# Performance work log

Hardware: AMD Instinct MI355X
Metric: run time of the kernel (lower is better)

Reference implementation:

```python
import jax, jax.numpy as jnp
import numpy as np

D_MODEL = 1024
D_HEAD = 64
N_HEADS = D_MODEL // D_HEAD
MAX_SEQ = 2048
BATCH = 2
SEQ = 2048


def setup_inputs() -> dict:
    key = jax.random.key(0)
    ks = jax.random.split(key, 10)
    s = 1.0 / np.sqrt(D_MODEL)
    return {
        "x": jax.random.normal(ks[0], (BATCH, SEQ, D_MODEL), dtype=jnp.float32),
        "Wq": jax.random.normal(ks[1], (D_MODEL, D_MODEL), dtype=jnp.float32) * s,
        "bq": jax.random.normal(ks[2], (D_MODEL,), dtype=jnp.float32) * 0.01,
        "Wk": jax.random.normal(ks[3], (D_MODEL, D_MODEL), dtype=jnp.float32) * s,
        "bk": jax.random.normal(ks[4], (D_MODEL,), dtype=jnp.float32) * 0.01,
        "Wv": jax.random.normal(ks[5], (D_MODEL, D_MODEL), dtype=jnp.float32) * s,
        "bv": jax.random.normal(ks[6], (D_MODEL,), dtype=jnp.float32) * 0.01,
        "Er": jax.random.normal(ks[7], (MAX_SEQ, D_HEAD), dtype=jnp.float32),
        "Wo": jax.random.normal(ks[8], (D_MODEL, D_MODEL), dtype=jnp.float32) * s,
        "bo": jax.random.normal(ks[9], (D_MODEL,), dtype=jnp.float32) * 0.01,
    }


def _s_rel(q, Er):
    # q: [B,H,S,Dh]; use last S rows of Er (start = max_seq - seq)
    S = q.shape[2]
    Er_slice = Er[Er.shape[0] - S:, :]                  # [S, Dh]
    qE = jnp.einsum("bhsd,ld->bhsl", q, Er_slice)       # [B,H,S,S]
    padded = jnp.pad(qE, ((0, 0), (0, 0), (0, 0), (1, 0)))  # [B,H,S,S+1]
    B, H, S1, S2 = padded.shape
    padded = padded.reshape(B, H, S2, S1)               # skew trick
    return padded[:, :, 1:, :]                          # [B,H,S,S]


def reference(x, Wq, bq, Wk, bk, Wv, bv, Er, Wo, bo):
    B, S, _ = x.shape
    scale = 1.0 / np.sqrt(D_HEAD)
    # projections (torch Linear: x @ W.T + b)
    def proj(W, b):
        return (x @ W.T + b).reshape(B, S, N_HEADS, D_HEAD).transpose(0, 2, 1, 3)
    q = proj(Wq, bq)   # [B,H,S,Dh]
    k = proj(Wk, bk)
    v = proj(Wv, bv)
    qk = jnp.einsum("bhsd,bhtd->bhst", q, k)            # [B,H,S,S]
    logits = (qk + _s_rel(q, Er)) * scale
    causal = jnp.tril(jnp.ones((S, S), dtype=bool))
    masked = jnp.where(causal[None, None], logits, -1e9)
    attn = jax.nn.softmax(masked, axis=-1)
    out = jnp.einsum("bhst,bhtd->bhsd", attn, v)        # [B,H,S,Dh]
    out = out.transpose(0, 2, 1, 3).reshape(B, S, D_MODEL)
    return out @ Wo.T + bo
```

## Files before the change

kernel.cpp:

```cpp
#include <hip/hip_runtime.h>
#include <hip/hip_bf16.h>

typedef short v8s __attribute__((ext_vector_type(8)));
typedef float v4f __attribute__((ext_vector_type(4)));
typedef __hip_bfloat16 bf16;
typedef unsigned int u32;

#define MFMA(a, b, c) __builtin_amdgcn_mfma_f32_16x16x32_bf16(a, b, c, 0, 0, 0)

__device__ __forceinline__ void gload16(const bf16* g, bf16* l) {
    __builtin_amdgcn_global_load_lds(
        (const __attribute__((address_space(1))) u32*)(g),
        (__attribute__((address_space(3))) u32*)(l), 16, 0, 0);
}

__global__ __launch_bounds__(256) void cast_all(
    const float* __restrict__ x,  const float* __restrict__ wq,
    const float* __restrict__ wk, const float* __restrict__ wv,
    const float* __restrict__ wo, const float* __restrict__ er,
    bf16* __restrict__ xb,  bf16* __restrict__ wqb, bf16* __restrict__ wkb,
    bf16* __restrict__ wvb, bf16* __restrict__ wob, bf16* __restrict__ erb)
{
    const int r = blockIdx.y;
    const float* s; bf16* d; int n4;
    if      (r == 0) { s = x;  d = xb;  n4 = 1048576; }
    else if (r == 1) { s = wq; d = wqb; n4 = 262144;  }
    else if (r == 2) { s = wk; d = wkb; n4 = 262144;  }
    else if (r == 3) { s = wv; d = wvb; n4 = 262144;  }
    else if (r == 4) { s = wo; d = wob; n4 = 262144;  }
    else             { s = er; d = erb; n4 = 32768;   }
    const int i = blockIdx.x * 256 + threadIdx.x;
    if (i < n4) {
        const float4 v = ((const float4*)s)[i];
        bf16 t[4];
        t[0] = __float2bfloat16(v.x);
        t[1] = __float2bfloat16(v.y);
        t[2] = __float2bfloat16(v.z);
        t[3] = __float2bfloat16(v.w);
        ((uint2*)d)[i] = *(const uint2*)t;
    }
}

__global__ __launch_bounds__(256) void gemm_nt(
    const bf16* __restrict__ A, const bf16* __restrict__ W,
    const float* __restrict__ b0, const float* __restrict__ b1,
    const float* __restrict__ b2,
    bf16* __restrict__ oHM, bf16* __restrict__ Vt, float* __restrict__ outf)
{
    __shared__ bf16 As[2][128 * 64];
    __shared__ bf16 Bs[2][128 * 64];

    const int tid = threadIdx.x;
    const int w  = tid >> 6, l = tid & 63;
    const int lm = l & 15,  lq = l >> 4;
    const int wm = (w >> 1) * 64, wn = (w & 1) * 64;
    const int m0 = blockIdx.y * 128, n0 = blockIdx.x * 128;

    const int grow = l >> 3;
    const int gcol = ((l & 7) ^ grow) * 8;

    v4f acc[4][4];
#pragma unroll
    for (int i = 0; i < 4; ++i)
#pragma unroll
        for (int j = 0; j < 4; ++j) acc[i][j] = (v4f){0.f, 0.f, 0.f, 0.f};

    const int sw = (lm & 7) << 4;

    auto STAGE = [&](int p, int k0) {
#pragma unroll
        for (int q = 0; q < 4; ++q) {
            const int rr = w * 32 + q * 8;
            gload16(&A[(size_t)(m0 + rr + grow) * 1024 + k0 + gcol], &As[p][rr * 64]);
            gload16(&W[(size_t)(n0 + rr + grow) * 1024 + k0 + gcol], &Bs[p][rr * 64]);
        }
    };
    auto COMPUTE = [&](int p) {
#pragma unroll
        for (int kk = 0; kk < 2; ++kk) {
            v8s a[4], b[4];
            const int cb = (lq * 16 + kk * 64);
#pragma unroll
            for (int i = 0; i < 4; ++i) {
                const int row = wm + i * 16 + lm;
                a[i] = *(const v8s*)((const char*)As[p] + row * 128 + (cb ^ sw));
            }
#pragma unroll
            for (int j = 0; j < 4; ++j) {
                const int row = wn + j * 16 + lm;
                b[j] = *(const v8s*)((const char*)Bs[p] + row * 128 + (cb ^ sw));
            }
#pragma unroll
            for (int i = 0; i < 4; ++i)
#pragma unroll
                for (int j = 0; j < 4; ++j)
                    acc[i][j] = MFMA(b[j], a[i], acc[i][j]);
        }
    };

    STAGE(0, 0);
    __syncthreads();
    for (int t = 0; t < 15; ++t) {
        STAGE((t + 1) & 1, (t + 1) * 64);
        COMPUTE(t & 1);
        __syncthreads();
    }
    COMPUTE(1);

    const int z = blockIdx.x >> 3;
    const float* bias = (z == 0) ? b0 : (z == 1) ? b1 : b2;

    float4 bj[4];
#pragma unroll
    for (int j = 0; j < 4; ++j)
        bj[j] = *(const float4*)&bias[(n0 & 1023) + wn + j * 16 + lq * 4];

#pragma unroll
    for (int i = 0; i < 4; ++i) {
        const int row = m0 + wm + i * 16 + lm;
        const int bb = row >> 11, ss = row & 2047;
#pragma unroll
        for (int j = 0; j < 4; ++j) {
            const int cc = (n0 & 1023) + wn + j * 16 + lq * 4;
            const float v0 = acc[i][j][0] + bj[j].x;
            const float v1 = acc[i][j][1] + bj[j].y;
            const float v2 = acc[i][j][2] + bj[j].z;
            const float v3 = acc[i][j][3] + bj[j].w;
            if (outf) {
                const float4 fv = {v0, v1, v2, v3};
                *(float4*)&outf[(size_t)row * 1024 + cc] = fv;
            } else {
                bf16 t[4];
                t[0] = __float2bfloat16(v0);
                t[1] = __float2bfloat16(v1);
                t[2] = __float2bfloat16(v2);
                t[3] = __float2bfloat16(v3);
                const int hh = cc >> 6, dd = cc & 63;
                if (z < 2) {
                    *(uint2*)&oHM[(size_t)z * 4194304 +
                        ((size_t)(bb * 16 + hh) * 2048 + ss) * 64 + dd] = *(uint2*)t;
                } else {
#pragma unroll
                    for (int r = 0; r < 4; ++r)
                        Vt[((size_t)(bb * 16 + hh) * 64 + dd + r) * 2048 + ss] = t[r];
                }
            }
        }
    }
}

__device__ const unsigned char QBt[48] = {
    31,31,30,15, 30,29,29,28,14, 28,27,27,26,13, 26,25,25,24,12,
    24,23,23,22,11, 22,21,21,20,10, 20,19,19,18,9, 18,17,17,16,8,
    16,7, 6,5,4,3,2,1,0};
__device__ const unsigned char TTt[48] = {
     0, 1, 0, 2,  1, 0, 1, 0, 2,  1, 0, 1, 0, 2,  1, 0, 1, 0, 2,
     1, 0, 1, 0, 2,  1, 0, 1, 0, 2,  1, 0, 1, 0, 2,  1, 0, 1, 0, 2,
     1, 2, 2,2,2,2,2,2,2};

__global__ __launch_bounds__(256, 4) void attn(
    const bf16* __restrict__ Q, const bf16* __restrict__ K,
    const bf16* __restrict__ Vt, const bf16* __restrict__ Er,
    bf16* __restrict__ AO, float* __restrict__ Opart, float* __restrict__ dpart)
{
    __shared__ bf16 Ks[64 * 72];
    __shared__ bf16 Vs[64 * 72];
    __shared__ bf16 Ps[64 * 72];
    __shared__ bf16 Gs2[64 * 100];

    const int ord = blockIdx.x;
    const int bh = ord & 31;
    const int s  = ord >> 5;
    const int qb = QBt[s];
    const int tt = TTt[s];
    const int t0   = (tt == 2) ? 0 : tt;
    const int step = (tt == 2) ? 1 : 2;
    const int slot = (tt == 2) ? -1 : (((qb - 16) * 32 + bh) * 2 + tt);

    const int i0 = qb * 64;
    const int b  = bh >> 4, h = bh & 15;
    const int tid = threadIdx.x;
    const int w  = tid >> 6, l = tid & 63;
    const int lm = l & 15,  lq = l >> 4;

    const bf16* qp = Q + ((size_t)bh * 2048 + i0 + w * 16 + lm) * 64 + lq * 8;
    const v8s q0 = *(const v8s*)qp;
    const v8s q1f = *(const v8s*)(qp + 32);

    v4f accO[4];
#pragma unroll
    for (int dt = 0; dt < 4; ++dt) accO[dt] = (v4f){0.f, 0.f, 0.f, 0.f};
    float rsc = 0.f;

    const int sr0 = tid >> 3;
    const int sc8 = (tid & 7) * 8;
    const size_t kbase = (size_t)bh * 2048 * 64;
    const size_t vbase = (size_t)bh * 64 * 2048;

    const int grow_g = (w * 16 + lm) * 100;
    const int prow   = (w * 16 + lm) * 72;
    const int ig     = i0 + w * 16 + lm;

    const int jt0 = t0 * 64;
    uint4 kp0 = *(const uint4*)&K[kbase + (size_t)(jt0 + sr0) * 64 + sc8];
    uint4 kp1 = *(const uint4*)&K[kbase + (size_t)(jt0 + sr0 + 32) * 64 + sc8];
    uint4 vp0 = *(const uint4*)&Vt[vbase + (size_t)sr0 * 2048 + jt0 + sc8];
    uint4 vp1 = *(const uint4*)&Vt[vbase + (size_t)(sr0 + 32) * 2048 + jt0 + sc8];

    for (int it = t0; it <= qb; it += step) {
        const int j0 = it * 64;
        __syncthreads();
        *(uint4*)&Ks[sr0 * 72 + sc8]        = kp0;
        *(uint4*)&Ks[(sr0 + 32) * 72 + sc8] = kp1;
        *(uint4*)&Vs[sr0 * 72 + sc8]        = vp0;
        *(uint4*)&Vs[(sr0 + 32) * 72 + sc8] = vp1;
        if (it + step <= qb) {
            const int jn = j0 + step * 64;
            kp0 = *(const uint4*)&K[kbase + (size_t)(jn + sr0) * 64 + sc8];
            kp1 = *(const uint4*)&K[kbase + (size_t)(jn + sr0 + 32) * 64 + sc8];
            vp0 = *(const uint4*)&Vt[vbase + (size_t)sr0 * 2048 + jn + sc8];
            vp1 = *(const uint4*)&Vt[vbase + (size_t)(sr0 + 32) * 2048 + jn + sc8];
        }
        const int basew = 2048 - 16 - i0 + j0 - 16 * w;
#pragma unroll
        for (int ct2 = 0; ct2 < 5; ++ct2) {
            int mr = basew + ct2 * 16 + lm;
            mr = (mr > 2047) ? 2047 : mr;
            const bf16* ep = Er + (size_t)mr * 64 + lq * 8;
            const v8s e0 = *(const v8s*)ep;
            const v8s e1 = *(const v8s*)(ep + 32);
            v4f g = (v4f){0.f, 0.f, 0.f, 0.f};
            g = MFMA(e0, q0, g);
            g = MFMA(e1, q1f, g);
            const int cb = ct2 * 16 + lq * 4 + lm + 1;
#pragma unroll
            for (int r = 0; r < 4; ++r)
                Gs2[grow_g + cb + r] = __float2bfloat16(g[r] * 0.125f);
        }
        __syncthreads();
        v4f sv[4];
#pragma unroll
        for (int ct = 0; ct < 4; ++ct) {
            const v8s k0f = *(const v8s*)&Ks[(ct * 16 + lm) * 72 + lq * 8];
            const v8s k1f = *(const v8s*)&Ks[(ct * 16 + lm) * 72 + 32 + lq * 8];
            v4f s2 = (v4f){0.f, 0.f, 0.f, 0.f};
            s2 = MFMA(k0f, q0, s2);
            s2 = MFMA(k1f, q1f, s2);
            sv[ct] = s2;
        }
#pragma unroll
        for (int ct = 0; ct < 4; ++ct) {
            const uint2 graw = *(const uint2*)&Gs2[grow_g + 16 + ct * 16 + lq * 4];
            const bf16* gb4 = (const bf16*)&graw;
            bf16 pt[4];
#pragma unroll
            for (int r = 0; r < 4; ++r) {
                const int jj = ct * 16 + lq * 4 + r;
                float sc = fmaf(sv[ct][r], 0.125f, (float)gb4[r]);
                if (j0 + jj > ig) sc = -1e9f;
                const float pe = __expf(sc - 4.0f);
                rsc += pe;
                pt[r] = __float2bfloat16(pe);
            }
            *(uint2*)&Ps[prow + ct * 16 + lq * 4] = *(const uint2*)pt;
        }
        const v8s pa0 = *(const v8s*)&Ps[prow + lq * 8];
        const v8s pa1 = *(const v8s*)&Ps[prow + 32 + lq * 8];
#pragma unroll
        for (int dt = 0; dt < 4; ++dt) {
            const v8s vb0 = *(const v8s*)&Vs[(dt * 16 + lm) * 72 + lq * 8];
            const v8s vb1 = *(const v8s*)&Vs[(dt * 16 + lm) * 72 + 32 + lq * 8];
            accO[dt] = MFMA(pa0, vb0, accO[dt]);
            accO[dt] = MFMA(pa1, vb1, accO[dt]);
        }
    }
    rsc += __shfl_xor(rsc, 16, 64);
    rsc += __shfl_xor(rsc, 32, 64);
    float den[4];
#pragma unroll
    for (int r = 0; r < 4; ++r) den[r] = __shfl(rsc, lq * 4 + r, 64);

    if (slot < 0) {
#pragma unroll
        for (int dt = 0; dt < 4; ++dt) {
#pragma unroll
            for (int r = 0; r < 4; ++r) {
                const int row = i0 + w * 16 + lq * 4 + r;
                const int d   = dt * 16 + lm;
                const float v = accO[dt][r] / den[r];
                AO[((size_t)b * 2048 + row) * 1024 + h * 64 + d] = __float2bfloat16(v);
            }
        }
    } else {
        float* op = Opart + (size_t)slot * 4096;
#pragma unroll
        for (int dt = 0; dt < 4; ++dt) {
#pragma unroll
            for (int r = 0; r < 4; ++r) {
                const int row = w * 16 + lq * 4 + r;
                op[row * 64 + dt * 16 + lm] = accO[dt][r];
            }
        }
        if (lm == 0) {
#pragma unroll
            for (int r = 0; r < 4; ++r)
                dpart[slot * 64 + w * 16 + lq * 4 + r] = den[r];
        }
    }
}

__global__ __launch_bounds__(256) void fixup(
    const float* __restrict__ Opart, const float* __restrict__ dpart,
    bf16* __restrict__ AO)
{
    const int pi = blockIdx.x;
    const int qb = 16 + (pi >> 5);
    const int bh = pi & 31;
    const int b = bh >> 4, h = bh & 15;
    const int t = threadIdx.x;
    const int row = t >> 2;
    const int c0 = (t & 3) * 16;
    const float dA = dpart[(pi * 2) * 64 + row];
    const float dB = dpart[(pi * 2 + 1) * 64 + row];
    const float inv = 1.0f / (dA + dB);
    const float* A = Opart + (size_t)(pi * 2) * 4096 + row * 64 + c0;
    const float* B = Opart + (size_t)(pi * 2 + 1) * 4096 + row * 64 + c0;
    bf16* dst = AO + ((size_t)b * 2048 + qb * 64 + row) * 1024 + h * 64 + c0;
#pragma unroll
    for (int c = 0; c < 16; c += 4) {
        bf16 tt[4];
#pragma unroll
        for (int r = 0; r < 4; ++r)
            tt[r] = __float2bfloat16((A[c + r] + B[c + r]) * inv);
        *(uint2*)&dst[c] = *(uint2*)tt;
    }
}

extern "C" void kernel_launch(void* const* d_in, const int* in_sizes, int n_in,
                              void* d_out, int out_size, void* d_ws, size_t ws_size,
                              hipStream_t stream)
{
    const float* x  = (const float*)d_in[0];
    const float* Wq = (const float*)d_in[1];
    const float* bq = (const float*)d_in[2];
    const float* Wk = (const float*)d_in[3];
    const float* bk = (const float*)d_in[4];
    const float* Wv = (const float*)d_in[5];
    const float* bv = (const float*)d_in[6];
    const float* Er = (const float*)d_in[7];
    const float* Wo = (const float*)d_in[8];
    const float* bo = (const float*)d_in[9];
    float* out = (float*)d_out;

    bf16* ws = (bf16*)d_ws;
    const size_t NEl = (size_t)4096 * 1024;
    bf16* Qw  = ws;
    bf16* Kw  = ws + NEl;
    bf16* Vtw = ws + 3 * NEl;
    bf16* xb  = ws + 4 * NEl;
    bf16* AOw = xb;
    bf16* Wqb = ws + 5 * NEl;
    bf16* Wkb = Wqb + 1024 * 1024;
    bf16* Wvb = Wkb + 1024 * 1024;
    bf16* Wob = Wvb + 1024 * 1024;
    bf16* Erb = Wob + 1024 * 1024;
    float* dpart = (float*)(Erb + (size_t)2048 * 64);
    float* Opart = out;
    (void)Kw;

    cast_all<<<dim3(4096, 6), 256, 0, stream>>>(x, Wq, Wk, Wv, Wo, Er,
                                                xb, Wqb, Wkb, Wvb, Wob, Erb);
    gemm_nt<<<dim3(24, 32), 256, 0, stream>>>(xb, Wqb, bq, bk, bv, Qw, Vtw, nullptr);
    attn<<<dim3(1536), 256, 0, stream>>>(Qw, Kw, Vtw, Erb, AOw, Opart, dpart);
    fixup<<<dim3(512), 256, 0, stream>>>(Opart, dpart, AOw);
    gemm_nt<<<dim3(8, 32), 256, 0, stream>>>(AOw, Wob, bo, bo, bo, nullptr, nullptr, out);
}
```

Baseline: 273.7 us.

## Read K and V fragments directly from global memory, drop LDS staging

Removes the K/V shared-memory tiles and their register prefetch, so each wave loads its MFMA operand fragments for K and Vt straight from global memory (served by cache). This frees LDS and registers and removes one barrier per iteration, and launch bounds are raised to allow 6 blocks per CU for more occupancy. The cost is that the four waves now each fetch the same K/V data redundantly through the cache hierarchy, and the loads are no longer prefetched one iteration ahead, so latency may be exposed.

```diff
diff --git a/kernel.cpp b/kernel.cpp
--- a/kernel.cpp
+++ b/kernel.cpp
@@ -158,13 +158,11 @@
      1, 0, 1, 0, 2,  1, 0, 1, 0, 2,  1, 0, 1, 0, 2,  1, 0, 1, 0, 2,
      1, 2, 2,2,2,2,2,2,2};
 
-__global__ __launch_bounds__(256, 4) void attn(
+__global__ __launch_bounds__(256, 6) void attn(
     const bf16* __restrict__ Q, const bf16* __restrict__ K,
     const bf16* __restrict__ Vt, const bf16* __restrict__ Er,
     bf16* __restrict__ AO, float* __restrict__ Opart, float* __restrict__ dpart)
 {
-    __shared__ bf16 Ks[64 * 72];
-    __shared__ bf16 Vs[64 * 72];
     __shared__ bf16 Ps[64 * 72];
     __shared__ bf16 Gs2[64 * 100];
 
@@ -192,8 +190,6 @@
     for (int dt = 0; dt < 4; ++dt) accO[dt] = (v4f){0.f, 0.f, 0.f, 0.f};
     float rsc = 0.f;
 
-    const int sr0 = tid >> 3;
-    const int sc8 = (tid & 7) * 8;
     const size_t kbase = (size_t)bh * 2048 * 64;
     const size_t vbase = (size_t)bh * 64 * 2048;
 
@@ -201,26 +197,8 @@
     const int prow   = (w * 16 + lm) * 72;
     const int ig     = i0 + w * 16 + lm;
 
-    const int jt0 = t0 * 64;
-    uint4 kp0 = *(const uint4*)&K[kbase + (size_t)(jt0 + sr0) * 64 + sc8];
-    uint4 kp1 = *(const uint4*)&K[kbase + (size_t)(jt0 + sr0 + 32) * 64 + sc8];
-    uint4 vp0 = *(const uint4*)&Vt[vbase + (size_t)sr0 * 2048 + jt0 + sc8];
-    uint4 vp1 = *(const uint4*)&Vt[vbase + (size_t)(sr0 + 32) * 2048 + jt0 + sc8];
-
     for (int it = t0; it <= qb; it += step) {
         const int j0 = it * 64;
-        __syncthreads();
-        *(uint4*)&Ks[sr0 * 72 + sc8]        = kp0;
-        *(uint4*)&Ks[(sr0 + 32) * 72 + sc8] = kp1;
-        *(uint4*)&Vs[sr0 * 72 + sc8]        = vp0;
-        *(uint4*)&Vs[(sr0 + 32) * 72 + sc8] = vp1;
-        if (it + step <= qb) {
-            const int jn = j0 + step * 64;
-            kp0 = *(const uint4*)&K[kbase + (size_t)(jn + sr0) * 64 + sc8];
-            kp1 = *(const uint4*)&K[kbase + (size_t)(jn + sr0 + 32) * 64 + sc8];
-            vp0 = *(const uint4*)&Vt[vbase + (size_t)sr0 * 2048 + jn + sc8];
-            vp1 = *(const uint4*)&Vt[vbase + (size_t)(sr0 + 32) * 2048 + jn + sc8];
-        }
         const int basew = 2048 - 16 - i0 + j0 - 16 * w;
 #pragma unroll
         for (int ct2 = 0; ct2 < 5; ++ct2) {
@@ -241,8 +219,9 @@
         v4f sv[4];
 #pragma unroll
         for (int ct = 0; ct < 4; ++ct) {
-            const v8s k0f = *(const v8s*)&Ks[(ct * 16 + lm) * 72 + lq * 8];
-            const v8s k1f = *(const v8s*)&Ks[(ct * 16 + lm) * 72 + 32 + lq * 8];
+            const bf16* kp = &K[kbase + (size_t)(j0 + ct * 16 + lm) * 64 + lq * 8];
+            const v8s k0f = *(const v8s*)kp;
+            const v8s k1f = *(const v8s*)(kp + 32);
             v4f s2 = (v4f){0.f, 0.f, 0.f, 0.f};
             s2 = MFMA(k0f, q0, s2);
             s2 = MFMA(k1f, q1f, s2);
@@ -268,11 +247,13 @@
         const v8s pa1 = *(const v8s*)&Ps[prow + 32 + lq * 8];
 #pragma unroll
         for (int dt = 0; dt < 4; ++dt) {
-            const v8s vb0 = *(const v8s*)&Vs[(dt * 16 + lm) * 72 + lq * 8];
-            const v8s vb1 = *(const v8s*)&Vs[(dt * 16 + lm) * 72 + 32 + lq * 8];
+            const bf16* vp = &Vt[vbase + (size_t)(dt * 16 + lm) * 2048 + j0 + lq * 8];
+            const v8s vb0 = *(const v8s*)vp;
+            const v8s vb1 = *(const v8s*)(vp + 32);
             accO[dt] = MFMA(pa0, vb0, accO[dt]);
             accO[dt] = MFMA(pa1, vb1, accO[dt]);
         }
+        asm volatile("" ::: "memory");
     }
     rsc += __shfl_xor(rsc, 16, 64);
     rsc += __shfl_xor(rsc, 32, 64);
@@ -287,8 +268,8 @@
             for (int r = 0; r < 4; ++r) {
                 const int row = i0 + w * 16 + lq * 4 + r;
                 const int d   = dt * 16 + lm;
-                const float v = accO[dt][r] / den[r];
-                AO[((size_t)b * 2048 + row) * 1024 + h * 64 + d] = __float2bfloat16(v);
+                AO[((size_t)b * 2048 + row) * 1024 + h * 64 + d] =
+                    __float2bfloat16(accO[dt][r] / den[r]);
             }
         }
     } else {
```

Result: slower. 374.1 us (+36.7%).
